# Kernel tuning notes

Hardware: AMD Instinct MI355X
Metric: run time of the kernel (lower is better)

The kernel has to match this reference:

```python
import jax, jax.numpy as jnp
import numpy as np

N, E, R, B, DIN, H1, H2 = 50000, 1000000, 8, 30, 64, 64, 64


def setup_inputs() -> dict:
    key = jax.random.key(0)
    ks = jax.random.split(key, 12)
    node_features = jax.random.normal(ks[0], (N, DIN), dtype=jnp.float32)
    src = jax.random.randint(ks[1], (E,), 0, N)
    dst = jax.random.randint(ks[2], (E,), 0, N)
    edge_index = jnp.stack([src, dst]).astype(jnp.int64)
    edge_norm = jax.random.uniform(ks[3], (E,), dtype=jnp.float32)
    edge_type = jax.random.randint(ks[4], (E,), 0, R).astype(jnp.int64)
    s = 0.05  # param init scale
    basis = jax.random.normal(ks[5], (B, DIN, H1), dtype=jnp.float32) * s
    comp = jax.random.normal(ks[6], (R, B), dtype=jnp.float32) * s
    loop_weight = jax.random.normal(ks[7], (DIN, H1), dtype=jnp.float32) * s
    bias1 = jnp.zeros((H1,), dtype=jnp.float32)
    weight2 = jax.random.normal(ks[8], (H1, H2), dtype=jnp.float32) * s
    bias2 = jnp.zeros((H2,), dtype=jnp.float32)
    return dict(node_features=node_features, edge_index=edge_index,
                edge_norm=edge_norm, edge_type=edge_type, basis=basis,
                comp=comp, loop_weight=loop_weight, bias1=bias1,
                weight2=weight2, bias2=bias2)


def reference(node_features, edge_index, edge_norm, edge_type, basis, comp,
              loop_weight, bias1, weight2, bias2):
    n = node_features.shape[0]
    src, dst = edge_index[0], edge_index[1]

    # ---- RGCNConv (basis decomposition, sum aggregation, self-loop, bias) ----
    # relation weights from bases: [R, DIN, H1]
    Wrel = jnp.einsum('rb,bio->rio', comp, basis)
    # transform every node by every relation once: [N, R, H1]
    xr = jnp.einsum('ni,rio->nro', node_features, Wrel)
    # per-edge message via (src, edge_type) gather: [E, H1]
    msg = xr[src, edge_type]
    agg1 = jax.ops.segment_sum(msg, dst, num_segments=n)
    h = agg1 + node_features @ loop_weight + bias1

    # ---- GraphConv (symmetric 'both' normalization) ----
    ones = jnp.ones((src.shape[0],), dtype=h.dtype)
    deg_out = jnp.clip(jax.ops.segment_sum(ones, src, num_segments=n), 1.0, None)
    deg_in = jnp.clip(jax.ops.segment_sum(ones, dst, num_segments=n), 1.0, None)
    hs = h * jax.lax.rsqrt(deg_out)[:, None]
    agg2 = jax.ops.segment_sum(hs[src], dst, num_segments=n)
    agg2 = agg2 * jax.lax.rsqrt(deg_in)[:, None]
    out = agg2 @ weight2 + bias2
    return out
```

## Files before the change

kernel.cpp:

```cpp
#include <hip/hip_runtime.h>

#define N_NODES 50000
#define N_EDGES 1000000
#define NB      128
#define CHUNK   7813
#define NQ      8
#define QN      6256
#define NBLK2   196

#define A_PART    0
#define A_XR      0
#define A_Y2      0
#define A_XBF     57600000
#define A_DEGP    115200000
#define A_ROWPTR  115400000
#define A_BSUM    115600128
#define A_BBASE   115601024
#define A_CSR     115601920
#define A_HS      123601920
#define A_WALL    136401920
typedef unsigned int uint32;
typedef unsigned short ushort16;
typedef __attribute__((ext_vector_type(8))) short bf16x8;
typedef __attribute__((ext_vector_type(4))) float f32x4;

__device__ inline ushort16 f2bf(float f) {
    uint32 u = __float_as_uint(f);
    return (ushort16)((u + 0x7FFFu + ((u >> 16) & 1u)) >> 16);
}
__device__ inline float bf2f(ushort16 h) {
    return __uint_as_float(((uint32)h) << 16);
}

__global__ void k_wall(const float* __restrict__ comp, const float* __restrict__ basis,
                       const float* __restrict__ loopw, ushort16* __restrict__ wallbf) {
    int idx = blockIdx.x * 256 + threadIdx.x;
    if (idx >= 9 * 4096) return;
    int r = idx >> 12, io = idx & 4095;
    int i = io >> 6, o = io & 63;
    float acc;
    if (r < 8) {
        acc = 0.f;
        #pragma unroll
        for (int b = 0; b < 30; ++b) acc += comp[r * 30 + b] * basis[b * 4096 + io];
    } else {
        acc = loopw[io];
    }
    wallbf[r * 4096 + o * 64 + i] = f2bf(acc);
}

__global__ __launch_bounds__(256) void k_xbf(const float* __restrict__ x,
                                             ushort16* __restrict__ xbf) {
    int g = blockIdx.x * 256 + threadIdx.x;
    int base = g * 8;
    if (base >= N_NODES * 64) return;
    float4 v0 = *(const float4*)&x[base];
    float4 v1 = *(const float4*)&x[base + 4];
    uint4 o;
    o.x = (uint32)f2bf(v0.x) | ((uint32)f2bf(v0.y) << 16);
    o.y = (uint32)f2bf(v0.z) | ((uint32)f2bf(v0.w) << 16);
    o.z = (uint32)f2bf(v1.x) | ((uint32)f2bf(v1.y) << 16);
    o.w = (uint32)f2bf(v1.z) | ((uint32)f2bf(v1.w) << 16);
    *(uint4*)&xbf[base] = o;
}

__global__ __launch_bounds__(256) void k_hist2(const int* __restrict__ ei,
                                               uint32* __restrict__ part) {
    __shared__ __align__(16) uint32 h[QN];
    int t = threadIdx.x, b = blockIdx.x, q = blockIdx.y;
    int lo = q * QN;
    int nq = N_NODES - lo; if (nq > QN) nq = QN;
    int4* h4 = (int4*)h;
    for (int i = t; i < QN / 4; i += 256) h4[i] = make_int4(0, 0, 0, 0);
    __syncthreads();
    int e0 = b * CHUNK, e1 = e0 + CHUNK;
    if (e1 > N_EDGES) e1 = N_EDGES;
    for (int e = e0 + t; e < e1; e += 256) {
        int s = ei[e], d = ei[N_EDGES + e];
        unsigned rs = (unsigned)(s - lo), rd = (unsigned)(d - lo);
        if (rs < (unsigned)QN) atomicAdd(&h[rs], 1u);
        if (rd < (unsigned)QN) atomicAdd(&h[rd], 0x10000u);
    }
    __syncthreads();
    int4* d4 = (int4*)(part + b * N_NODES + lo);
    const int4* s4 = (const int4*)h;
    for (int i = t; i < nq / 4; i += 256) d4[i] = s4[i];
}

__global__ __launch_bounds__(256) void k_merge(const uint32* __restrict__ part,
                                               uint32* __restrict__ degp,
                                               int* __restrict__ bsum) {
    int t = threadIdx.x, v = blockIdx.x * 256 + t;
    uint32 s = 0;
    if (v < N_NODES) {
        #pragma unroll 8
        for (int b = 0; b < NB; ++b) s += part[b * N_NODES + v];
        degp[v] = s;
    }
    int din = (int)(s >> 16);
    int r = din;
    #pragma unroll
    for (int d = 1; d < 64; d <<= 1) r += __shfl_xor(r, d);
    __shared__ int wsum[4];
    int lane = t & 63, wid = t >> 6;
    if (lane == 0) wsum[wid] = r;
    __syncthreads();
    if (t == 0) bsum[blockIdx.x] = wsum[0] + wsum[1] + wsum[2] + wsum[3];
}

__global__ void k_scanb(const int* __restrict__ bsum, int* __restrict__ bbase) {
    int t = threadIdx.x;
    int v = (t < NBLK2) ? bsum[t] : 0;
    int lane = t & 63, wid = t >> 6;
    int x = v;
    #pragma unroll
    for (int d = 1; d < 64; d <<= 1) {
        int y = __shfl_up(x, d);
        if (lane >= d) x += y;
    }
    __shared__ int wsum[4];
    if (lane == 63) wsum[wid] = x;
    __syncthreads();
    int base = 0;
    for (int w = 0; w < wid; ++w) base += wsum[w];
    if (t < NBLK2) bbase[t] = base + x - v;
}

__global__ __launch_bounds__(256) void k_base(uint32* __restrict__ part,
                                              const uint32* __restrict__ degp,
                                              const int* __restrict__ bbase,
                                              int* __restrict__ rowptr) {
    int t = threadIdx.x, v = blockIdx.x * 256 + t;
    int din = (v < N_NODES) ? (int)(degp[v] >> 16) : 0;
    int lane = t & 63, wid = t >> 6;
    int x = din;
    #pragma unroll
    for (int d = 1; d < 64; d <<= 1) {
        int y = __shfl_up(x, d);
        if (lane >= d) x += y;
    }
    __shared__ int wsum[4];
    if (lane == 63) wsum[wid] = x;
    __syncthreads();
    int base = bbase[blockIdx.x];
    for (int w = 0; w < wid; ++w) base += wsum[w];
    int start = base + x - din;
    if (v < N_NODES) {
        rowptr[v] = start;
        if (v == N_NODES - 1) rowptr[N_NODES] = start + din;
        uint32 run = (uint32)start;
        for (int b = 0; b < NB; ++b) {
            uint32 p = part[b * N_NODES + v];
            part[b * N_NODES + v] = run;
            run += (p >> 16);
        }
    }
}

__global__ __launch_bounds__(256) void k_fill2(const int* __restrict__ ei,
                                               const int* __restrict__ etype,
                                               const uint32* __restrict__ fillbase,
                                               uint32* __restrict__ csr) {
    __shared__ __align__(16) uint32 cur[QN];
    int t = threadIdx.x, q = blockIdx.x, b = blockIdx.y;
    int lo = q * QN;
    int nq = N_NODES - lo; if (nq > QN) nq = QN;
    const int4* s4 = (const int4*)(fillbase + b * N_NODES + lo);
    int4* c4 = (int4*)cur;
    for (int i = t; i < nq / 4; i += 256) c4[i] = s4[i];
    __syncthreads();
    int e0 = b * CHUNK, e1 = e0 + CHUNK;
    if (e1 > N_EDGES) e1 = N_EDGES;
    for (int e = e0 + t; e < e1; e += 256) {
        int d = ei[N_EDGES + e];
        unsigned rd = (unsigned)(d - lo);
        if (rd < (unsigned)QN) {
            int s = ei[e], ty = etype[e];
            uint32 pos = atomicAdd(&cur[rd], 1u);
            csr[pos] = (uint32)(s * 9 + ty);
        }
    }
}

__global__ __launch_bounds__(256) void k_xr(const ushort16* __restrict__ xbf,
                                            const ushort16* __restrict__ wallbf,
                                            ushort16* __restrict__ xr) {
    __shared__ __align__(16) ushort16 Abf[64 * 64];
    __shared__ __align__(16) ushort16 Wbf[64 * 64];
    __shared__ __align__(16) ushort16 Ot[64 * 64];
    int t = threadIdx.x;
    int n0 = blockIdx.x * 64;
    int r = blockIdx.y;
    {
        int n = t >> 2, s0 = (t & 3) * 2;
        uint4 v0 = make_uint4(0, 0, 0, 0), v1 = v0;
        if (n0 + n < N_NODES) {
            v0 = *(const uint4*)&xbf[(n0 + n) * 64 + s0 * 8];
            v1 = *(const uint4*)&xbf[(n0 + n) * 64 + s0 * 8 + 8];
        }
        *(uint4*)&Abf[n * 64 + ((s0 ^ (n & 7)) * 8)]       = v0;
        *(uint4*)&Abf[n * 64 + (((s0 + 1) ^ (n & 7)) * 8)] = v1;
        uint4 w0 = *(const uint4*)&wallbf[r * 4096 + n * 64 + s0 * 8];
        uint4 w1 = *(const uint4*)&wallbf[r * 4096 + n * 64 + s0 * 8 + 8];
        *(uint4*)&Wbf[n * 64 + ((s0 ^ (n & 7)) * 8)]       = w0;
        *(uint4*)&Wbf[n * 64 + (((s0 + 1) ^ (n & 7)) * 8)] = w1;
    }
    __syncthreads();
    int w = t >> 6, l = t & 63;
    int row = l & 15, kg = l >> 4;
    int an = w * 16 + row;
    bf16x8 a0 = *(const bf16x8*)&Abf[an * 64 + (((0 + kg) ^ (an & 7)) * 8)];
    bf16x8 a1 = *(const bf16x8*)&Abf[an * 64 + (((4 + kg) ^ (an & 7)) * 8)];
    #pragma unroll
    for (int ct = 0; ct < 4; ++ct) {
        int bo = ct * 16 + row;
        bf16x8 b0 = *(const bf16x8*)&Wbf[bo * 64 + (((0 + kg) ^ (bo & 7)) * 8)];
        bf16x8 b1 = *(const bf16x8*)&Wbf[bo * 64 + (((4 + kg) ^ (bo & 7)) * 8)];
        f32x4 acc = {0.f, 0.f, 0.f, 0.f};
        acc = __builtin_amdgcn_mfma_f32_16x16x32_bf16(a0, b0, acc, 0, 0, 0);
        acc = __builtin_amdgcn_mfma_f32_16x16x32_bf16(a1, b1, acc, 0, 0, 0);
        #pragma unroll
        for (int j = 0; j < 4; ++j)
            Ot[(w * 16 + kg * 4 + j) * 64 + ct * 16 + row] = f2bf(acc[j]);
    }
    __syncthreads();
    {
        int n = t >> 2, s = (t & 3) * 2;
        if (n0 + n < N_NODES) {
            *(uint4*)&xr[(n0 + n) * 576 + r * 64 + s * 8] =
                *(const uint4*)&Ot[n * 64 + s * 8];
            *(uint4*)&xr[(n0 + n) * 576 + r * 64 + s * 8 + 8] =
                *(const uint4*)&Ot[n * 64 + s * 8 + 8];
        }
    }
}

__global__ __launch_bounds__(256) void k_agg1(const ushort16* __restrict__ xr,
                                              const uint32* __restrict__ csr,
                                              const int* __restrict__ rowptr,
                                              const uint32* __restrict__ degp,
                                              const float* __restrict__ bias1,
                                              ushort16* __restrict__ hs) {
    int t = threadIdx.x;
    int wid = t >> 6, lane = t & 63;
    int v = blockIdx.x * 4 + wid;
    if (v >= N_NODES) return;
    int sub = lane >> 4, cg = lane & 15;
    float a0 = 0.f, a1 = 0.f, a2 = 0.f, a3 = 0.f;
    int end = rowptr[v + 1];
    for (int j = rowptr[v] + sub; j < end; j += 4) {
        uint32 r0 = csr[j];
        uint2 u = *(const uint2*)&xr[r0 * 64 + cg * 4];
        a0 += __uint_as_float(u.x << 16);
        a1 += __uint_as_float(u.x & 0xffff0000u);
        a2 += __uint_as_float(u.y << 16);
        a3 += __uint_as_float(u.y & 0xffff0000u);
    }
    #pragma unroll
    for (int d = 16; d < 64; d <<= 1) {
        a0 += __shfl_xor(a0, d);
        a1 += __shfl_xor(a1, d);
        a2 += __shfl_xor(a2, d);
        a3 += __shfl_xor(a3, d);
    }
    uint2 slu = *(const uint2*)&xr[(v * 9 + 8) * 64 + cg * 4];
    float4 b = *(const float4*)&bias1[cg * 4];
    a0 += __uint_as_float(slu.x << 16) + b.x;
    a1 += __uint_as_float(slu.x & 0xffff0000u) + b.y;
    a2 += __uint_as_float(slu.y << 16) + b.z;
    a3 += __uint_as_float(slu.y & 0xffff0000u) + b.w;
    float dg = (float)(degp[v] & 0xffffu);
    if (dg < 1.f) dg = 1.f;
    float s = rsqrtf(dg);
    if (sub == 0) {
        uint2 o;
        o.x = (uint32)f2bf(a0 * s) | ((uint32)f2bf(a1 * s) << 16);
        o.y = (uint32)f2bf(a2 * s) | ((uint32)f2bf(a3 * s) << 16);
        *(uint2*)&hs[v * 64 + cg * 4] = o;
    }
}

__global__ __launch_bounds__(256) void k_agg2(const ushort16* __restrict__ hs,
                                              const uint32* __restrict__ csr,
                                              const int* __restrict__ rowptr,
                                              const uint32* __restrict__ degp,
                                              float* __restrict__ y2) {
    int t = threadIdx.x;
    int wid = t >> 6, lane = t & 63;
    int v = blockIdx.x * 4 + wid;
    if (v >= N_NODES) return;
    int sub = lane >> 4, cg = lane & 15;
    float a0 = 0.f, a1 = 0.f, a2 = 0.f, a3 = 0.f;
    int end = rowptr[v + 1];
    for (int j = rowptr[v] + sub; j < end; j += 4) {
        uint32 r0 = csr[j] / 9u;
        uint2 u = *(const uint2*)&hs[r0 * 64 + cg * 4];
        a0 += __uint_as_float(u.x << 16);
        a1 += __uint_as_float(u.x & 0xffff0000u);
        a2 += __uint_as_float(u.y << 16);
        a3 += __uint_as_float(u.y & 0xffff0000u);
    }
    #pragma unroll
    for (int d = 16; d < 64; d <<= 1) {
        a0 += __shfl_xor(a0, d);
        a1 += __shfl_xor(a1, d);
        a2 += __shfl_xor(a2, d);
        a3 += __shfl_xor(a3, d);
    }
    float dg = (float)(degp[v] >> 16);
    if (dg < 1.f) dg = 1.f;
    float s = rsqrtf(dg);
    if (sub == 0) {
        *(float4*)&y2[v * 64 + cg * 4] =
            make_float4(a0 * s, a1 * s, a2 * s, a3 * s);
    }
}

__global__ __launch_bounds__(256) void k_gemm2(const float* __restrict__ y2,
                                               const float* __restrict__ w2,
                                               const float* __restrict__ bias2,
                                               float* __restrict__ out) {
    __shared__ __align__(16) float At[32 * 256];
    __shared__ __align__(16) float Wt[32 * 64];
    int t = threadIdx.x;
    int n0 = blockIdx.x * 256;
    int og = t & 7, ng = t >> 3;
    float acc[8][8];
    #pragma unroll
    for (int i = 0; i < 8; ++i)
        #pragma unroll
        for (int j = 0; j < 8; ++j) acc[i][j] = 0.f;

    #pragma unroll
    for (int ph = 0; ph < 2; ++ph) {
        if (ph) __syncthreads();
        #pragma unroll
        for (int j = 0; j < 8; ++j) {
            int f4 = t + j * 256;
            int n = f4 >> 3, k4 = f4 & 7;
            float4 v = make_float4(0.f, 0.f, 0.f, 0.f);
            if (n0 + n < N_NODES)
                v = *(const float4*)&y2[(n0 + n) * 64 + ph * 32 + k4 * 4];
            int sl = n >> 2, nl = n & 3, kb = k4 * 4;
            At[(kb + 0) * 256 + (((sl ^ ((kb + 0) & 7)) << 2) | nl)] = v.x;
            At[(kb + 1) * 256 + (((sl ^ ((kb + 1) & 7)) << 2) | nl)] = v.y;
            At[(kb + 2) * 256 + (((sl ^ ((kb + 2) & 7)) << 2) | nl)] = v.z;
            At[(kb + 3) * 256 + (((sl ^ ((kb + 3) & 7)) << 2) | nl)] = v.w;
        }
        #pragma unroll
        for (int j = 0; j < 8; ++j) {
            int f = t + j * 256;
            Wt[f] = w2[ph * 2048 + f];
        }
        __syncthreads();
        #pragma unroll 4
        for (int k = 0; k < 32; ++k) {
            int c = k & 7;
            float4 aA = *(const float4*)&At[k * 256 + (((2 * ng) ^ c) << 2)];
            float4 aB = *(const float4*)&At[k * 256 + (((2 * ng + 1) ^ c) << 2)];
            float4 w0 = *(const float4*)&Wt[k * 64 + og * 8];
            float4 w1 = *(const float4*)&Wt[k * 64 + og * 8 + 4];
            float a_[8] = {aA.x, aA.y, aA.z, aA.w, aB.x, aB.y, aB.z, aB.w};
            float w_[8] = {w0.x, w0.y, w0.z, w0.w, w1.x, w1.y, w1.z, w1.w};
            #pragma unroll
            for (int i = 0; i < 8; ++i)
                #pragma unroll
                for (int j = 0; j < 8; ++j) acc[i][j] += a_[i] * w_[j];
        }
    }
    float4 b0 = *(const float4*)&bias2[og * 8];
    float4 b1 = *(const float4*)&bias2[og * 8 + 4];
    #pragma unroll
    for (int i = 0; i < 8; ++i) {
        int n = n0 + ng * 8 + i;
        if (n < N_NODES) {
            *(float4*)&out[n * 64 + og * 8] =
                make_float4(acc[i][0] + b0.x, acc[i][1] + b0.y,
                            acc[i][2] + b0.z, acc[i][3] + b0.w);
            *(float4*)&out[n * 64 + og * 8 + 4] =
                make_float4(acc[i][4] + b1.x, acc[i][5] + b1.y,
                            acc[i][6] + b1.z, acc[i][7] + b1.w);
        }
    }
}

extern "C" void kernel_launch(void* const* d_in, const int* in_sizes, int n_in,
                              void* d_out, int out_size, void* d_ws, size_t ws_size,
                              hipStream_t stream) {
    const float* x      = (const float*)d_in[0];
    const int*   ei     = (const int*)d_in[1];
    const int*   etype  = (const int*)d_in[3];
    const float* basis  = (const float*)d_in[4];
    const float* comp   = (const float*)d_in[5];
    const float* loopw  = (const float*)d_in[6];
    const float* bias1  = (const float*)d_in[7];
    const float* w2     = (const float*)d_in[8];
    const float* bias2  = (const float*)d_in[9];
    float* out = (float*)d_out;

    char* ws = (char*)d_ws;
    uint32*   part   = (uint32*)(ws + A_PART);
    ushort16* xr     = (ushort16*)(ws + A_XR);
    float*    y2     = (float*)(ws + A_Y2);
    ushort16* xbf    = (ushort16*)(ws + A_XBF);
    uint32*   degp   = (uint32*)(ws + A_DEGP);
    int*      rowptr = (int*)(ws + A_ROWPTR);
    int*      bsum   = (int*)(ws + A_BSUM);
    int*      bbase  = (int*)(ws + A_BBASE);
    uint32*   csr    = (uint32*)(ws + A_CSR);
    ushort16* hs     = (ushort16*)(ws + A_HS);
    ushort16* wallbf = (ushort16*)(ws + A_WALL);

    k_wall<<<144, 256, 0, stream>>>(comp, basis, loopw, wallbf);
    k_xbf<<<(N_NODES * 64 / 8 + 255) / 256, 256, 0, stream>>>(x, xbf);
    k_hist2<<<dim3(NB, NQ), 256, 0, stream>>>(ei, part);
    k_merge<<<NBLK2, 256, 0, stream>>>(part, degp, bsum);
    k_scanb<<<1, 256, 0, stream>>>(bsum, bbase);
    k_base<<<NBLK2, 256, 0, stream>>>(part, degp, bbase, rowptr);
    k_fill2<<<dim3(NQ, NB), 256, 0, stream>>>(ei, etype, part, csr);
    k_xr<<<dim3((N_NODES + 63) / 64, 9), 256, 0, stream>>>(xbf, wallbf, xr);
    k_agg1<<<N_NODES / 4, 256, 0, stream>>>(xr, csr, rowptr, degp, bias1, hs);
    k_agg2<<<N_NODES / 4, 256, 0, stream>>>(hs, csr, rowptr, degp, y2);
    k_gemm2<<<(N_NODES + 255) / 256, 256, 0, stream>>>(y2, w2, bias2, out);
}
```

Baseline: 256.5 us.

## Aggregate raw features per relation before transform instead of transforming all nodes

Replaces the transform-then-gather scheme, which computed xr for all 9 relations and gathered 128-byte rows per edge, with aggregate-then-transform. Neighbor features are first summed into a per-node, per-relation buffer S using LDS atomics. A single GEMM over K=9×64 then applies the relation weights, bias and degree normalization. The per-edge gather now reads from the smaller xbf table, but the change adds LDS float atomics, a 576-wide S write and read, and rounds the partial sums to bf16 before the GEMM.

```diff
diff --git a/kernel.cpp b/kernel.cpp
--- a/kernel.cpp
+++ b/kernel.cpp
@@ -9,7 +9,7 @@
 #define NBLK2   196
 
 #define A_PART    0
-#define A_XR      0
+#define A_S       0
 #define A_Y2      0
 #define A_XBF     57600000
 #define A_DEGP    115200000
@@ -182,101 +182,120 @@
     }
 }
 
-__global__ __launch_bounds__(256) void k_xr(const ushort16* __restrict__ xbf,
-                                            const ushort16* __restrict__ wallbf,
-                                            ushort16* __restrict__ xr) {
+__global__ __launch_bounds__(256) void k_aggS(const ushort16* __restrict__ xbf,
+                                              const uint32* __restrict__ csr,
+                                              const int* __restrict__ rowptr,
+                                              ushort16* __restrict__ S) {
+    __shared__ float Sl[4 * 576];
+    int t = threadIdx.x;
+    int wid = t >> 6, lane = t & 63;
+    int v = blockIdx.x * 4 + wid;
+    for (int i = t; i < 4 * 576; i += 256) Sl[i] = 0.f;
+    __syncthreads();
+    int sub = lane >> 4, cg = lane & 15;
+    float* Sw = &Sl[wid * 576];
+    if (v < N_NODES) {
+        int end = rowptr[v + 1];
+        for (int j = rowptr[v] + sub; j < end; j += 4) {
+            uint32 e = csr[j];
+            uint32 src = e / 9u;
+            int ty = (int)(e - src * 9u);
+            uint2 u = *(const uint2*)&xbf[src * 64 + cg * 4];
+            atomicAdd(&Sw[ty * 64 + cg * 4 + 0], __uint_as_float(u.x << 16));
+            atomicAdd(&Sw[ty * 64 + cg * 4 + 1], __uint_as_float(u.x & 0xffff0000u));
+            atomicAdd(&Sw[ty * 64 + cg * 4 + 2], __uint_as_float(u.y << 16));
+            atomicAdd(&Sw[ty * 64 + cg * 4 + 3], __uint_as_float(u.y & 0xffff0000u));
+        }
+    }
+    __syncthreads();
+    if (v < N_NODES && sub == 0) {
+        uint2 u = *(const uint2*)&xbf[(uint32)v * 64 + cg * 4];
+        Sw[8 * 64 + cg * 4 + 0] += __uint_as_float(u.x << 16);
+        Sw[8 * 64 + cg * 4 + 1] += __uint_as_float(u.x & 0xffff0000u);
+        Sw[8 * 64 + cg * 4 + 2] += __uint_as_float(u.y << 16);
+        Sw[8 * 64 + cg * 4 + 3] += __uint_as_float(u.y & 0xffff0000u);
+    }
+    __syncthreads();
+    if (v < N_NODES) {
+        uint32* Sg = (uint32*)S + (size_t)v * 288;
+        #pragma unroll
+        for (int i = lane; i < 288; i += 64) {
+            Sg[i] = (uint32)f2bf(Sw[2 * i]) | ((uint32)f2bf(Sw[2 * i + 1]) << 16);
+        }
+    }
+}
+
+__global__ __launch_bounds__(256) void k_gemm1(const ushort16* __restrict__ S,
+                                               const ushort16* __restrict__ wallbf,
+                                               const uint32* __restrict__ degp,
+                                               const float* __restrict__ bias1,
+                                               ushort16* __restrict__ hs) {
     __shared__ __align__(16) ushort16 Abf[64 * 64];
     __shared__ __align__(16) ushort16 Wbf[64 * 64];
     __shared__ __align__(16) ushort16 Ot[64 * 64];
     int t = threadIdx.x;
     int n0 = blockIdx.x * 64;
-    int r = blockIdx.y;
-    {
-        int n = t >> 2, s0 = (t & 3) * 2;
-        uint4 v0 = make_uint4(0, 0, 0, 0), v1 = v0;
-        if (n0 + n < N_NODES) {
-            v0 = *(const uint4*)&xbf[(n0 + n) * 64 + s0 * 8];
-            v1 = *(const uint4*)&xbf[(n0 + n) * 64 + s0 * 8 + 8];
-        }
-        *(uint4*)&Abf[n * 64 + ((s0 ^ (n & 7)) * 8)]       = v0;
-        *(uint4*)&Abf[n * 64 + (((s0 + 1) ^ (n & 7)) * 8)] = v1;
-        uint4 w0 = *(const uint4*)&wallbf[r * 4096 + n * 64 + s0 * 8];
-        uint4 w1 = *(const uint4*)&wallbf[r * 4096 + n * 64 + s0 * 8 + 8];
-        *(uint4*)&Wbf[n * 64 + ((s0 ^ (n & 7)) * 8)]       = w0;
-        *(uint4*)&Wbf[n * 64 + (((s0 + 1) ^ (n & 7)) * 8)] = w1;
-    }
-    __syncthreads();
     int w = t >> 6, l = t & 63;
     int row = l & 15, kg = l >> 4;
-    int an = w * 16 + row;
-    bf16x8 a0 = *(const bf16x8*)&Abf[an * 64 + (((0 + kg) ^ (an & 7)) * 8)];
-    bf16x8 a1 = *(const bf16x8*)&Abf[an * 64 + (((4 + kg) ^ (an & 7)) * 8)];
+    f32x4 acc0 = {0.f, 0.f, 0.f, 0.f}, acc1 = acc0, acc2 = acc0, acc3 = acc0;
+    for (int r = 0; r < 9; ++r) {
+        if (r) __syncthreads();
+        {
+            int n = t >> 2, s0 = (t & 3) * 2;
+            uint4 v0 = make_uint4(0, 0, 0, 0), v1 = v0;
+            if (n0 + n < N_NODES) {
+                const ushort16* srcp = &S[(size_t)(n0 + n) * 576 + r * 64];
+                v0 = *(const uint4*)&srcp[s0 * 8];
+                v1 = *(const uint4*)&srcp[s0 * 8 + 8];
+            }
+            *(uint4*)&Abf[n * 64 + ((s0 ^ (n & 7)) * 8)]       = v0;
+            *(uint4*)&Abf[n * 64 + (((s0 + 1) ^ (n & 7)) * 8)] = v1;
+            uint4 w0 = *(const uint4*)&wallbf[r * 4096 + n * 64 + s0 * 8];
+            uint4 w1 = *(const uint4*)&wallbf[r * 4096 + n * 64 + s0 * 8 + 8];
+            *(uint4*)&Wbf[n * 64 + ((s0 ^ (n & 7)) * 8)]       = w0;
+            *(uint4*)&Wbf[n * 64 + (((s0 + 1) ^ (n & 7)) * 8)] = w1;
+        }
+        __syncthreads();
+        int an = w * 16 + row;
+        bf16x8 a0 = *(const bf16x8*)&Abf[an * 64 + (((0 + kg) ^ (an & 7)) * 8)];
+        bf16x8 a1 = *(const bf16x8*)&Abf[an * 64 + (((4 + kg) ^ (an & 7)) * 8)];
+        #pragma unroll
+        for (int ct = 0; ct < 4; ++ct) {
+            int bo = ct * 16 + row;
+            bf16x8 b0 = *(const bf16x8*)&Wbf[bo * 64 + (((0 + kg) ^ (bo & 7)) * 8)];
+            bf16x8 b1 = *(const bf16x8*)&Wbf[bo * 64 + (((4 + kg) ^ (bo & 7)) * 8)];
+            f32x4 a_in = (ct == 0) ? acc0 : (ct == 1) ? acc1 : (ct == 2) ? acc2 : acc3;
+            f32x4 a_out = __builtin_amdgcn_mfma_f32_16x16x32_bf16(a0, b0, a_in, 0, 0, 0);
+            a_out = __builtin_amdgcn_mfma_f32_16x16x32_bf16(a1, b1, a_out, 0, 0, 0);
+            if (ct == 0) acc0 = a_out; else if (ct == 1) acc1 = a_out;
+            else if (ct == 2) acc2 = a_out; else acc3 = a_out;
+        }
+    }
     #pragma unroll
     for (int ct = 0; ct < 4; ++ct) {
-        int bo = ct * 16 + row;
-        bf16x8 b0 = *(const bf16x8*)&Wbf[bo * 64 + (((0 + kg) ^ (bo & 7)) * 8)];
-        bf16x8 b1 = *(const bf16x8*)&Wbf[bo * 64 + (((4 + kg) ^ (bo & 7)) * 8)];
-        f32x4 acc = {0.f, 0.f, 0.f, 0.f};
-        acc = __builtin_amdgcn_mfma_f32_16x16x32_bf16(a0, b0, acc, 0, 0, 0);
-        acc = __builtin_amdgcn_mfma_f32_16x16x32_bf16(a1, b1, acc, 0, 0, 0);
-        #pragma unroll
-        for (int j = 0; j < 4; ++j)
-            Ot[(w * 16 + kg * 4 + j) * 64 + ct * 16 + row] = f2bf(acc[j]);
+        f32x4 a = (ct == 0) ? acc0 : (ct == 1) ? acc1 : (ct == 2) ? acc2 : acc3;
+        float b = bias1[ct * 16 + row];
+        #pragma unroll
+        for (int j = 0; j < 4; ++j) {
+            int node = w * 16 + kg * 4 + j;
+            int gv = n0 + node;
+            float dg = 1.f;
+            if (gv < N_NODES) {
+                dg = (float)(degp[gv] & 0xffffu);
+                if (dg < 1.f) dg = 1.f;
+            }
+            Ot[node * 64 + ct * 16 + row] = f2bf((a[j] + b) * rsqrtf(dg));
+        }
     }
     __syncthreads();
     {
         int n = t >> 2, s = (t & 3) * 2;
         if (n0 + n < N_NODES) {
-            *(uint4*)&xr[(n0 + n) * 576 + r * 64 + s * 8] =
+            *(uint4*)&hs[(n0 + n) * 64 + s * 8] =
                 *(const uint4*)&Ot[n * 64 + s * 8];
-            *(uint4*)&xr[(n0 + n) * 576 + r * 64 + s * 8 + 8] =
+            *(uint4*)&hs[(n0 + n) * 64 + s * 8 + 8] =
                 *(const uint4*)&Ot[n * 64 + s * 8 + 8];
         }
-    }
-}
-
-__global__ __launch_bounds__(256) void k_agg1(const ushort16* __restrict__ xr,
-                                              const uint32* __restrict__ csr,
-                                              const int* __restrict__ rowptr,
-                                              const uint32* __restrict__ degp,
-                                              const float* __restrict__ bias1,
-                                              ushort16* __restrict__ hs) {
-    int t = threadIdx.x;
-    int wid = t >> 6, lane = t & 63;
-    int v = blockIdx.x * 4 + wid;
-    if (v >= N_NODES) return;
-    int sub = lane >> 4, cg = lane & 15;
-    float a0 = 0.f, a1 = 0.f, a2 = 0.f, a3 = 0.f;
-    int end = rowptr[v + 1];
-    for (int j = rowptr[v] + sub; j < end; j += 4) {
-        uint32 r0 = csr[j];
-        uint2 u = *(const uint2*)&xr[r0 * 64 + cg * 4];
-        a0 += __uint_as_float(u.x << 16);
-        a1 += __uint_as_float(u.x & 0xffff0000u);
-        a2 += __uint_as_float(u.y << 16);
-        a3 += __uint_as_float(u.y & 0xffff0000u);
-    }
-    #pragma unroll
-    for (int d = 16; d < 64; d <<= 1) {
-        a0 += __shfl_xor(a0, d);
-        a1 += __shfl_xor(a1, d);
-        a2 += __shfl_xor(a2, d);
-        a3 += __shfl_xor(a3, d);
-    }
-    uint2 slu = *(const uint2*)&xr[(v * 9 + 8) * 64 + cg * 4];
-    float4 b = *(const float4*)&bias1[cg * 4];
-    a0 += __uint_as_float(slu.x << 16) + b.x;
-    a1 += __uint_as_float(slu.x & 0xffff0000u) + b.y;
-    a2 += __uint_as_float(slu.y << 16) + b.z;
-    a3 += __uint_as_float(slu.y & 0xffff0000u) + b.w;
-    float dg = (float)(degp[v] & 0xffffu);
-    if (dg < 1.f) dg = 1.f;
-    float s = rsqrtf(dg);
-    if (sub == 0) {
-        uint2 o;
-        o.x = (uint32)f2bf(a0 * s) | ((uint32)f2bf(a1 * s) << 16);
-        o.y = (uint32)f2bf(a2 * s) | ((uint32)f2bf(a3 * s) << 16);
-        *(uint2*)&hs[v * 64 + cg * 4] = o;
     }
 }
 
@@ -400,7 +419,7 @@
 
     char* ws = (char*)d_ws;
     uint32*   part   = (uint32*)(ws + A_PART);
-    ushort16* xr     = (ushort16*)(ws + A_XR);
+    ushort16* S      = (ushort16*)(ws + A_S);
     float*    y2     = (float*)(ws + A_Y2);
     ushort16* xbf    = (ushort16*)(ws + A_XBF);
     uint32*   degp   = (uint32*)(ws + A_DEGP);
@@ -418,8 +437,8 @@
     k_scanb<<<1, 256, 0, stream>>>(bsum, bbase);
     k_base<<<NBLK2, 256, 0, stream>>>(part, degp, bbase, rowptr);
     k_fill2<<<dim3(NQ, NB), 256, 0, stream>>>(ei, etype, part, csr);
-    k_xr<<<dim3((N_NODES + 63) / 64, 9), 256, 0, stream>>>(xbf, wallbf, xr);
-    k_agg1<<<N_NODES / 4, 256, 0, stream>>>(xr, csr, rowptr, degp, bias1, hs);
+    k_aggS<<<N_NODES / 4, 256, 0, stream>>>(xbf, csr, rowptr, S);
+    k_gemm1<<<(N_NODES + 63) / 64, 256, 0, stream>>>(S, wallbf, degp, bias1, hs);
     k_agg2<<<N_NODES / 4, 256, 0, stream>>>(hs, csr, rowptr, degp, y2);
     k_gemm2<<<(N_NODES + 255) / 256, 256, 0, stream>>>(y2, w2, bias2, out);
 }
```

Result: slower. 558.1 us (+117.6%).
